# Kernel optimization log

Measured on AMD Instinct MI355X. Metric: run time of the kernel, lower is better.

The kernel has to match this reference:

```python
import math
import jax, jax.numpy as jnp
import numpy as np

B, T, C, H = 2, 2048, 1024, 16

def setup_inputs() -> dict:
    key = jax.random.key(0)
    k1, k2, k3 = jax.random.split(key, 3)
    x = jax.random.normal(k1, (B, T, C), dtype=jnp.float32)
    W_kqv = jax.random.normal(k2, (C, 3 * C), dtype=jnp.float32) * (1.0 / math.sqrt(C))
    W_proj = jax.random.normal(k3, (C, C), dtype=jnp.float32) * (1.0 / math.sqrt(C))
    b_proj = jnp.zeros((C,), dtype=jnp.float32)
    return {"x": x, "W_kqv": W_kqv, "W_proj": W_proj, "b_proj": b_proj}

def reference(x, W_kqv, W_proj, b_proj):
    Bx, Tx, Cx = x.shape
    hs = Cx // H  # head size
    q, k, v = jnp.split(x @ W_kqv, 3, axis=2)  # each (B,T,C)
    # (B,T,C) -> (B,H,T,hs)
    q = q.reshape(Bx, Tx, H, hs).transpose(0, 2, 1, 3)
    k = k.reshape(Bx, Tx, H, hs).transpose(0, 2, 1, 3)
    v = v.reshape(Bx, Tx, H, hs).transpose(0, 2, 1, 3)
    attn = jnp.einsum('bhqd,bhkd->bhqk', q, k) / math.sqrt(hs)  # (B,H,T,T)
    causal = jnp.tril(jnp.ones((Tx, Tx), dtype=bool))
    attn = jnp.where(causal, attn, -jnp.inf)
    attn = jax.nn.softmax(attn, axis=-1)
    y = jnp.einsum('bhqk,bhkd->bhqd', attn, v)  # (B,H,T,hs)
    y = y.transpose(0, 2, 1, 3).reshape(Bx, Tx, Cx)
    return y @ W_proj + b_proj
```

## Files before the change

### kernel.cpp

```cpp
#include <hip/hip_runtime.h>


typedef unsigned short u16;
typedef unsigned int u32;
typedef __bf16 bf16x8 __attribute__((ext_vector_type(8)));
typedef float f32x4 __attribute__((ext_vector_type(4)));
typedef u32 u32x4 __attribute__((ext_vector_type(4)));
typedef u16 u16x4 __attribute__((ext_vector_type(4)));

__constant__ signed char JM[22] = {9,8,7,15,15,14,14,6,13,13,12,12,5,11,11,10,10,4,3,2,1,0};
__constant__ signed char JH[22] = {0,0,0,1, 2, 1, 2, 0,1, 2, 1, 2, 0,1, 2, 1, 2, 0,0,0,0,0};

__device__ __forceinline__ u16 f2bf(float f) {
  u32 u = __float_as_uint(f);
  u32 r = u + 0x7FFFu + ((u >> 16) & 1u);
  return (u16)(r >> 16);
}

__device__ __forceinline__ bf16x8 ld_bf8(const u16* p) {
  union { u32x4 u; bf16x8 b; } x;
  x.u = *(const u32x4*)p;
  return x.b;
}

__device__ __forceinline__ void gld_lds16(const u16* g, u16* l) {
  __builtin_amdgcn_global_load_lds(
      (const __attribute__((address_space(1))) u32*)g,
      (__attribute__((address_space(3))) u32*)l, 16, 0, 0);
}

__global__ __launch_bounds__(256) void conv_x_kernel(const float* __restrict__ src,
                                                     u16* __restrict__ dst) {
  int idx = blockIdx.x * 256 + threadIdx.x;
  const float4* s4 = (const float4*)src;
  float4 a = s4[2 * idx], b = s4[2 * idx + 1];
  union { u16 h[8]; u32x4 v; } pk;
  pk.h[0] = f2bf(a.x); pk.h[1] = f2bf(a.y); pk.h[2] = f2bf(a.z); pk.h[3] = f2bf(a.w);
  pk.h[4] = f2bf(b.x); pk.h[5] = f2bf(b.y); pk.h[6] = f2bf(b.z); pk.h[7] = f2bf(b.w);
  *(u32x4*)&dst[(size_t)idx * 8] = pk.v;
}

__global__ __launch_bounds__(256) void convT_kernel(const float* __restrict__ src,
                                                    u16* __restrict__ dst, int R, int Cc) {
  __shared__ float ls[64][65];
  int r0 = blockIdx.x * 64, c0 = blockIdx.y * 64;
  int t = threadIdx.x;
  for (int u = t; u < 1024; u += 256) {
    int r = u >> 4, cs = (u & 15) << 2;
    float4 v = *(const float4*)&src[(size_t)(r0 + r) * Cc + (c0 + cs)];
    ls[r][cs] = v.x; ls[r][cs + 1] = v.y; ls[r][cs + 2] = v.z; ls[r][cs + 3] = v.w;
  }
  __syncthreads();
  for (int u = t; u < 1024; u += 256) {
    int n = u >> 4, ks = (u & 15) << 2;
    u16x4 o;
    o.x = f2bf(ls[ks][n]); o.y = f2bf(ls[ks + 1][n]);
    o.z = f2bf(ls[ks + 2][n]); o.w = f2bf(ls[ks + 3][n]);
    *(u16x4*)&dst[(size_t)(c0 + n) * R + (r0 + ks)] = o;
  }
}

__global__ __launch_bounds__(256) void qkv_gemm_kernel(
    const u16* __restrict__ A, const u16* __restrict__ Bt,
    u16* __restrict__ Qh, u16* __restrict__ Kh, u16* __restrict__ Vh, float qscale) {
  constexpr int K = 1024;
  __shared__ __align__(16) u16 As[128 * 32];
  __shared__ __align__(16) u16 Bs[128 * 32];
  int t = threadIdx.x;
  int wave = t >> 6, lane = t & 63, quad = lane >> 4, l16 = lane & 15;
  int wm = (wave >> 1) << 6, wn = (wave & 1) << 6;
  int m0 = blockIdx.x * 128, n0 = blockIdx.y * 128;
  f32x4 acc[4][4] = {};
  int u0 = t, u1 = t + 256;
  int ra0 = u0 >> 2, ca0 = ((u0 & 3) ^ ((u0 >> 3) & 3)) << 3;
  int ra1 = u1 >> 2, ca1 = ((u1 & 3) ^ ((u1 >> 3) & 3)) << 3;
  int swq = (quad ^ ((l16 >> 1) & 3)) << 3;
  for (int k0 = 0; k0 < K; k0 += 32) {
    gld_lds16(&A[(size_t)(m0 + ra0) * K + k0 + ca0], &As[u0 * 8]);
    gld_lds16(&A[(size_t)(m0 + ra1) * K + k0 + ca1], &As[u1 * 8]);
    gld_lds16(&Bt[(size_t)(n0 + ra0) * K + k0 + ca0], &Bs[u0 * 8]);
    gld_lds16(&Bt[(size_t)(n0 + ra1) * K + k0 + ca1], &Bs[u1 * 8]);
    __syncthreads();
    bf16x8 af[4], bfr[4];
    for (int r = 0; r < 4; ++r) af[r] = ld_bf8(&As[(wm + r * 16 + l16) * 32 + swq]);
    for (int c = 0; c < 4; ++c) bfr[c] = ld_bf8(&Bs[(wn + c * 16 + l16) * 32 + swq]);
    for (int r = 0; r < 4; ++r)
      for (int c = 0; c < 4; ++c)
        acc[r][c] = __builtin_amdgcn_mfma_f32_16x16x32_bf16(af[r], bfr[c], acc[r][c], 0, 0, 0);
    __syncthreads();
  }
  for (int r = 0; r < 4; ++r) {
    int rowbase = m0 + wm + r * 16 + quad * 4;
    for (int c = 0; c < 4; ++c) {
      int col = n0 + wn + c * 16 + l16;
      int seg = col >> 10;
      int cc = col & 1023;
      int h = cc >> 6, d = cc & 63;
      for (int i = 0; i < 4; ++i) {
        int row = rowbase + i;
        int b = row >> 11, tt = row & 2047;
        size_t off = (((size_t)(b * 16 + h)) * 2048 + tt) * 64 + d;
        float v = acc[r][c][i];
        if (seg == 0)      Qh[off] = f2bf(v * qscale);
        else if (seg == 1) Kh[off] = f2bf(v);
        else               Vh[off] = f2bf(v);
      }
    }
  }
}

__global__ __launch_bounds__(256) void vT_kernel(const u16* __restrict__ Vh,
                                                 u16* __restrict__ Vt) {
  __shared__ __align__(16) u16 ls[64 * 72];
  int t = threadIdx.x;
  int t0 = blockIdx.x * 64, bh = blockIdx.y;
  const u16* in = Vh + ((size_t)bh * 2048 + t0) * 64;
  for (int u = t; u < 512; u += 256) {
    int row = u >> 3, col = (u & 7) << 3;
    *(u32x4*)&ls[row * 72 + col] = *(const u32x4*)&in[(size_t)row * 64 + col];
  }
  __syncthreads();
  for (int u = t; u < 512; u += 256) {
    int d = u >> 3, tc = (u & 7) << 3;
    union { u16 h[8]; u32x4 v; } pk;
    for (int j = 0; j < 8; ++j) pk.h[j] = ls[(tc + j) * 72 + d];
    *(u32x4*)&Vt[((size_t)bh * 64 + d) * 2048 + t0 + tc] = pk.v;
  }
}

__global__ __launch_bounds__(512) void proj_gemm_kernel(
    const u16* __restrict__ A, const u16* __restrict__ Bt,
    float* __restrict__ out, const float* __restrict__ bias) {
  constexpr int K = 1024;
  __shared__ __align__(16) u16 As[128 * 32];
  __shared__ __align__(16) u16 Bs[128 * 32];
  int t = threadIdx.x;
  int wave = t >> 6, lane = t & 63, quad = lane >> 4, l16 = lane & 15;
  int wm = (wave >> 2) << 6, wn = (wave & 3) << 5;
  int m0 = blockIdx.x * 128, n0 = blockIdx.y * 128;
  f32x4 acc[4][2] = {};
  int u0 = t;
  int ra0 = u0 >> 2, ca0 = ((u0 & 3) ^ ((u0 >> 3) & 3)) << 3;
  int swq = (quad ^ ((l16 >> 1) & 3)) << 3;
  for (int k0 = 0; k0 < K; k0 += 32) {
    gld_lds16(&A[(size_t)(m0 + ra0) * K + k0 + ca0], &As[u0 * 8]);
    gld_lds16(&Bt[(size_t)(n0 + ra0) * K + k0 + ca0], &Bs[u0 * 8]);
    __syncthreads();
    bf16x8 af[4], bfr[2];
    for (int r = 0; r < 4; ++r) af[r] = ld_bf8(&As[(wm + r * 16 + l16) * 32 + swq]);
    for (int c = 0; c < 2; ++c) bfr[c] = ld_bf8(&Bs[(wn + c * 16 + l16) * 32 + swq]);
    for (int r = 0; r < 4; ++r)
      for (int c = 0; c < 2; ++c)
        acc[r][c] = __builtin_amdgcn_mfma_f32_16x16x32_bf16(af[r], bfr[c], acc[r][c], 0, 0, 0);
    __syncthreads();
  }
  for (int r = 0; r < 4; ++r) {
    int rowbase = m0 + wm + r * 16 + quad * 4;
    for (int c = 0; c < 2; ++c) {
      int col = n0 + wn + c * 16 + l16;
      float bv = bias[col];
      for (int i = 0; i < 4; ++i)
        out[(size_t)(rowbase + i) * 1024 + col] = acc[r][c][i] + bv;
    }
  }
}

__global__ __launch_bounds__(256) void flash_kernel(
    const u16* __restrict__ Qh, const u16* __restrict__ Kh, const u16* __restrict__ Vt,
    u16* __restrict__ yb, float* __restrict__ Opart) {
  __shared__ __align__(16) u16 Ks[64 * 64];
  __shared__ __align__(16) u16 Vs[64 * 64];
  __shared__ __align__(16) u16 Ps[128 * 64];
  int t = threadIdx.x, wave = t >> 6, lane = t & 63, quad = lane >> 4, l16 = lane & 15;
  int jx = blockIdx.x, bh = blockIdx.y;
  int m = JM[jx], jh = JH[jx];
  int kvs = (jh == 2) ? (m + 1) : 0;
  int kve = (jh == 1) ? (m + 1) : (2 * m + 2);
  bool partial = jh != 0;
  int q0 = m << 7;
  const u16* Qb = Qh + (size_t)bh * 2048 * 64;
  const u16* Kb = Kh + (size_t)bh * 2048 * 64;
  const u16* Vb = Vt + (size_t)bh * 64 * 2048;
  bf16x8 qa[2][2];
  for (int s = 0; s < 2; ++s) {
    int qrow = q0 + wave * 32 + s * 16 + l16;
    qa[s][0] = ld_bf8(&Qb[(size_t)qrow * 64 + quad * 8]);
    qa[s][1] = ld_bf8(&Qb[(size_t)qrow * 64 + 32 + quad * 8]);
  }
  f32x4 oacc[2][4] = {};
  float ls0 = 0.f, ls1 = 0.f;
  int ua = t, ub = t + 256;
  int ra = ua >> 3, cba = ua & 7, rb = ub >> 3, cbb = ub & 7;
  int lka = ra * 64 + ((cba + ra) & 7) * 8;
  int lkb = rb * 64 + ((cbb + rb) & 7) * 8;
  u32x4 kreg0, kreg1, vreg0, vreg1;
  {
    int kv0 = kvs << 6;
    kreg0 = *(const u32x4*)&Kb[(size_t)(kv0 + ra) * 64 + cba * 8];
    kreg1 = *(const u32x4*)&Kb[(size_t)(kv0 + rb) * 64 + cbb * 8];
    vreg0 = *(const u32x4*)&Vb[(size_t)ra * 2048 + kv0 + cba * 8];
    vreg1 = *(const u32x4*)&Vb[(size_t)rb * 2048 + kv0 + cbb * 8];
  }
  for (int j = kvs; j < kve; ++j) {
    int kv0 = j << 6;
    __syncthreads();
    *(u32x4*)&Ks[lka] = kreg0;
    *(u32x4*)&Ks[lkb] = kreg1;
    *(u32x4*)&Vs[lka] = vreg0;
    *(u32x4*)&Vs[lkb] = vreg1;
    __syncthreads();
    if (j + 1 < kve) {
      int kn = (j + 1) << 6;
      kreg0 = *(const u32x4*)&Kb[(size_t)(kn + ra) * 64 + cba * 8];
      kreg1 = *(const u32x4*)&Kb[(size_t)(kn + rb) * 64 + cbb * 8];
      vreg0 = *(const u32x4*)&Vb[(size_t)ra * 2048 + kn + cba * 8];
      vreg1 = *(const u32x4*)&Vb[(size_t)rb * 2048 + kn + cbb * 8];
    }
    bool maskit = (j >= 2 * m);
    for (int c = 0; c < 4; ++c) {
      int krow = c * 16 + l16;
      bf16x8 kb0 = ld_bf8(&Ks[krow * 64 + ((quad + krow) & 7) * 8]);
      bf16x8 kb1 = ld_bf8(&Ks[krow * 64 + ((quad + 4 + krow) & 7) * 8]);
      for (int s = 0; s < 2; ++s) {
        f32x4 z = {0.f, 0.f, 0.f, 0.f};
        z = __builtin_amdgcn_mfma_f32_16x16x32_bf16(kb0, qa[s][0], z, 0, 0, 0);
        z = __builtin_amdgcn_mfma_f32_16x16x32_bf16(kb1, qa[s][1], z, 0, 0, 0);
        int prow = wave * 32 + s * 16 + l16;
        union { u16 hh[4]; u16x4 v; } pk;
        float lsadd = 0.f;
        for (int i = 0; i < 4; ++i) {
          float p = __builtin_amdgcn_exp2f(z[i]);
          if (maskit && (kv0 + c * 16 + quad * 4 + i > q0 + prow)) p = 0.f;
          lsadd += p;
          pk.hh[i] = f2bf(p);
        }
        if (s) ls1 += lsadd; else ls0 += lsadd;
        *(u16x4*)&Ps[prow * 64 + ((2 * c + (quad >> 1) + prow) & 7) * 8 + (quad & 1) * 4] = pk.v;
      }
    }
    bf16x8 pa[2][2];
    for (int s = 0; s < 2; ++s) {
      int prow = wave * 32 + s * 16 + l16;
      pa[s][0] = ld_bf8(&Ps[prow * 64 + ((quad + prow) & 7) * 8]);
      pa[s][1] = ld_bf8(&Ps[prow * 64 + ((quad + 4 + prow) & 7) * 8]);
    }
    for (int dt = 0; dt < 4; ++dt) {
      int vrow = dt * 16 + l16;
      bf16x8 vb0 = ld_bf8(&Vs[vrow * 64 + ((quad + vrow) & 7) * 8]);
      bf16x8 vb1 = ld_bf8(&Vs[vrow * 64 + ((quad + 4 + vrow) & 7) * 8]);
      for (int s = 0; s < 2; ++s) {
        oacc[s][dt] = __builtin_amdgcn_mfma_f32_16x16x32_bf16(pa[s][0], vb0, oacc[s][dt], 0, 0, 0);
        oacc[s][dt] = __builtin_amdgcn_mfma_f32_16x16x32_bf16(pa[s][1], vb1, oacc[s][dt], 0, 0, 0);
      }
    }
  }
  ls0 += __shfl_xor(ls0, 16); ls0 += __shfl_xor(ls0, 32);
  ls1 += __shfl_xor(ls1, 16); ls1 += __shfl_xor(ls1, 32);
  if (partial) {
    float* Op = Opart + ((size_t)(bh * 6 + (m - 10)) * 2 + (jh - 1)) * 8320;
    for (int s = 0; s < 2; ++s)
      for (int dt = 0; dt < 4; ++dt)
        for (int i = 0; i < 4; ++i)
          Op[(wave * 32 + s * 16 + quad * 4 + i) * 64 + dt * 16 + l16] = oacc[s][dt][i];
    if (quad == 0) {
      Op[8192 + wave * 32 + l16] = ls0;
      Op[8192 + wave * 32 + 16 + l16] = ls1;
    }
  } else {
    int b = bh >> 4, hh = bh & 15;
    for (int s = 0; s < 2; ++s) {
      float lss = s ? ls1 : ls0;
      for (int i = 0; i < 4; ++i) {
        float inv = 1.0f / __shfl(lss, quad * 4 + i);
        int qq = q0 + wave * 32 + s * 16 + quad * 4 + i;
        size_t rowoff = ((size_t)(b * 2048 + qq)) * 1024 + hh * 64;
        for (int dt = 0; dt < 4; ++dt)
          yb[rowoff + dt * 16 + l16] = f2bf(oacc[s][dt][i] * inv);
      }
    }
  }
}

__global__ __launch_bounds__(256) void combine_kernel(const float* __restrict__ Opart,
                                                      u16* __restrict__ yb) {
  int sx = blockIdx.x, bh = blockIdx.y, t = threadIdx.x;
  int m = 10 + sx;
  const float* A = Opart + (size_t)(bh * 6 + sx) * 2 * 8320;
  const float* Bp = A + 8320;
  int q = t >> 1, d0 = (t & 1) << 5;
  float inv = 1.0f / (A[8192 + q] + Bp[8192 + q]);
  int b = bh >> 4, h = bh & 15;
  size_t off = ((size_t)(b * 2048 + (m << 7) + q)) * 1024 + h * 64 + d0;
  for (int k0 = 0; k0 < 32; k0 += 8) {
    union { u16 hh[8]; u32x4 v; } pk;
    for (int k = 0; k < 8; ++k)
      pk.hh[k] = f2bf((A[q * 64 + d0 + k0 + k] + Bp[q * 64 + d0 + k0 + k]) * inv);
    *(u32x4*)&yb[off + k0] = pk.v;
  }
}

extern "C" void kernel_launch(void* const* d_in, const int* in_sizes, int n_in,
                              void* d_out, int out_size, void* d_ws, size_t ws_size,
                              hipStream_t stream) {
  const float* x     = (const float*)d_in[0];
  const float* Wkqv  = (const float*)d_in[1];
  const float* Wproj = (const float*)d_in[2];
  const float* bproj = (const float*)d_in[3];
  float* out = (float*)d_out;

  u16* ws     = (u16*)d_ws;
  u16* xb     = ws;
  u16* wkqvT  = xb + (size_t)4096 * 1024;
  u16* wprojT = wkqvT + (size_t)3072 * 1024;
  u16* Qh     = wprojT + (size_t)1024 * 1024;
  u16* Kh     = Qh + (size_t)32 * 2048 * 64;
  u16* Vt     = Kh + (size_t)32 * 2048 * 64;
  u16* yb     = Vt + (size_t)32 * 2048 * 64;
  u16* Vh     = yb;
  float* Opart = (float*)ws;

  const float QSCALE = 0.18033688011112042f;

  conv_x_kernel<<<2048, 256, 0, stream>>>(x, xb);
  convT_kernel<<<dim3(16, 48), 256, 0, stream>>>(Wkqv, wkqvT, 1024, 3072);
  convT_kernel<<<dim3(16, 16), 256, 0, stream>>>(Wproj, wprojT, 1024, 1024);
  qkv_gemm_kernel<<<dim3(32, 24), 256, 0, stream>>>(xb, wkqvT, Qh, Kh, Vh, QSCALE);
  vT_kernel<<<dim3(32, 32), 256, 0, stream>>>(Vh, Vt);
  flash_kernel<<<dim3(22, 32), 256, 0, stream>>>(Qh, Kh, Vt, yb, Opart);
  combine_kernel<<<dim3(6, 32), 256, 0, stream>>>(Opart, yb);
  proj_gemm_kernel<<<dim3(32, 8), 512, 0, stream>>>(yb, wprojT, out, bproj);
}
```

Measured before the change: 198.7 us.

## Split flash attention into single-wave 16-row query blocks with direct global K/V loads

The flash kernel moves from 256-thread blocks over 128 query rows, which staged K/V through shared memory with double-buffered registers, to 64-thread single-wave blocks over 16 query rows. Each wave loads K and V fragments straight from global memory, and the longest 64 row tiles are split in half along the KV axis, with a resized combine kernel merging the halves. The aim is finer load balancing over the causal triangle, no block-level barriers, and more concurrent blocks. In exchange, K/V global traffic rises sharply because each 16-row block re-reads its full K/V prefix without shared-memory reuse, and the global loads are no longer prefetched ahead of use.

```diff
diff --git a/kernel.cpp b/kernel.cpp
--- a/kernel.cpp
+++ b/kernel.cpp
@@ -7,9 +7,6 @@
 typedef float f32x4 __attribute__((ext_vector_type(4)));
 typedef u32 u32x4 __attribute__((ext_vector_type(4)));
 typedef u16 u16x4 __attribute__((ext_vector_type(4)));
-
-__constant__ signed char JM[22] = {9,8,7,15,15,14,14,6,13,13,12,12,5,11,11,10,10,4,3,2,1,0};
-__constant__ signed char JH[22] = {0,0,0,1, 2, 1, 2, 0,1, 2, 1, 2, 0,1, 2, 1, 2, 0,0,0,0,0};
 
 __device__ __forceinline__ u16 f2bf(float f) {
   u32 u = __float_as_uint(f);
@@ -165,138 +162,102 @@
   }
 }
 
-__global__ __launch_bounds__(256) void flash_kernel(
+__global__ __launch_bounds__(64, 4) void flash_kernel(
     const u16* __restrict__ Qh, const u16* __restrict__ Kh, const u16* __restrict__ Vt,
     u16* __restrict__ yb, float* __restrict__ Opart) {
-  __shared__ __align__(16) u16 Ks[64 * 64];
-  __shared__ __align__(16) u16 Vs[64 * 64];
-  __shared__ __align__(16) u16 Ps[128 * 64];
-  int t = threadIdx.x, wave = t >> 6, lane = t & 63, quad = lane >> 4, l16 = lane & 15;
+  __shared__ __align__(16) u16 Ps[16 * 64];
+  int t = threadIdx.x, quad = t >> 4, l16 = t & 15;
   int jx = blockIdx.x, bh = blockIdx.y;
-  int m = JM[jx], jh = JH[jx];
-  int kvs = (jh == 2) ? (m + 1) : 0;
-  int kve = (jh == 1) ? (m + 1) : (2 * m + 2);
-  bool partial = jh != 0;
-  int q0 = m << 7;
+  int s, kvs, kve, half = 0;
+  bool partial = false;
+  if (jx < 32) {
+    s = 95 - jx; kvs = 0; kve = (s >> 2) + 1;
+  } else if (jx < 96) {
+    int idx = jx - 32;
+    s = 96 + (idx >> 1); half = idx & 1;
+    int n = (s >> 2) + 1, mid = n >> 1;
+    kvs = half ? mid : 0; kve = half ? n : mid;
+    partial = true;
+  } else {
+    s = 159 - jx; kvs = 0; kve = (s >> 2) + 1;
+  }
+  int q0 = s << 4, smax = s >> 2;
   const u16* Qb = Qh + (size_t)bh * 2048 * 64;
   const u16* Kb = Kh + (size_t)bh * 2048 * 64;
   const u16* Vb = Vt + (size_t)bh * 64 * 2048;
-  bf16x8 qa[2][2];
-  for (int s = 0; s < 2; ++s) {
-    int qrow = q0 + wave * 32 + s * 16 + l16;
-    qa[s][0] = ld_bf8(&Qb[(size_t)qrow * 64 + quad * 8]);
-    qa[s][1] = ld_bf8(&Qb[(size_t)qrow * 64 + 32 + quad * 8]);
-  }
-  f32x4 oacc[2][4] = {};
-  float ls0 = 0.f, ls1 = 0.f;
-  int ua = t, ub = t + 256;
-  int ra = ua >> 3, cba = ua & 7, rb = ub >> 3, cbb = ub & 7;
-  int lka = ra * 64 + ((cba + ra) & 7) * 8;
-  int lkb = rb * 64 + ((cbb + rb) & 7) * 8;
-  u32x4 kreg0, kreg1, vreg0, vreg1;
-  {
-    int kv0 = kvs << 6;
-    kreg0 = *(const u32x4*)&Kb[(size_t)(kv0 + ra) * 64 + cba * 8];
-    kreg1 = *(const u32x4*)&Kb[(size_t)(kv0 + rb) * 64 + cbb * 8];
-    vreg0 = *(const u32x4*)&Vb[(size_t)ra * 2048 + kv0 + cba * 8];
-    vreg1 = *(const u32x4*)&Vb[(size_t)rb * 2048 + kv0 + cbb * 8];
-  }
+  bf16x8 qa0 = ld_bf8(&Qb[(size_t)(q0 + l16) * 64 + quad * 8]);
+  bf16x8 qa1 = ld_bf8(&Qb[(size_t)(q0 + l16) * 64 + 32 + quad * 8]);
+  f32x4 oacc[4] = {};
+  float lsum = 0.f;
   for (int j = kvs; j < kve; ++j) {
     int kv0 = j << 6;
-    __syncthreads();
-    *(u32x4*)&Ks[lka] = kreg0;
-    *(u32x4*)&Ks[lkb] = kreg1;
-    *(u32x4*)&Vs[lka] = vreg0;
-    *(u32x4*)&Vs[lkb] = vreg1;
-    __syncthreads();
-    if (j + 1 < kve) {
-      int kn = (j + 1) << 6;
-      kreg0 = *(const u32x4*)&Kb[(size_t)(kn + ra) * 64 + cba * 8];
-      kreg1 = *(const u32x4*)&Kb[(size_t)(kn + rb) * 64 + cbb * 8];
-      vreg0 = *(const u32x4*)&Vb[(size_t)ra * 2048 + kn + cba * 8];
-      vreg1 = *(const u32x4*)&Vb[(size_t)rb * 2048 + kn + cbb * 8];
-    }
-    bool maskit = (j >= 2 * m);
+    bf16x8 kb[4][2], vb[4][2];
     for (int c = 0; c < 4; ++c) {
-      int krow = c * 16 + l16;
-      bf16x8 kb0 = ld_bf8(&Ks[krow * 64 + ((quad + krow) & 7) * 8]);
-      bf16x8 kb1 = ld_bf8(&Ks[krow * 64 + ((quad + 4 + krow) & 7) * 8]);
-      for (int s = 0; s < 2; ++s) {
-        f32x4 z = {0.f, 0.f, 0.f, 0.f};
-        z = __builtin_amdgcn_mfma_f32_16x16x32_bf16(kb0, qa[s][0], z, 0, 0, 0);
-        z = __builtin_amdgcn_mfma_f32_16x16x32_bf16(kb1, qa[s][1], z, 0, 0, 0);
-        int prow = wave * 32 + s * 16 + l16;
-        union { u16 hh[4]; u16x4 v; } pk;
-        float lsadd = 0.f;
-        for (int i = 0; i < 4; ++i) {
-          float p = __builtin_amdgcn_exp2f(z[i]);
-          if (maskit && (kv0 + c * 16 + quad * 4 + i > q0 + prow)) p = 0.f;
-          lsadd += p;
-          pk.hh[i] = f2bf(p);
-        }
-        if (s) ls1 += lsadd; else ls0 += lsadd;
-        *(u16x4*)&Ps[prow * 64 + ((2 * c + (quad >> 1) + prow) & 7) * 8 + (quad & 1) * 4] = pk.v;
+      const u16* kp = &Kb[(size_t)(kv0 + c * 16 + l16) * 64 + quad * 8];
+      kb[c][0] = ld_bf8(kp);
+      kb[c][1] = ld_bf8(kp + 32);
+    }
+    for (int dt = 0; dt < 4; ++dt) {
+      const u16* vp = &Vb[(size_t)(dt * 16 + l16) * 2048 + kv0 + quad * 8];
+      vb[dt][0] = ld_bf8(vp);
+      vb[dt][1] = ld_bf8(vp + 32);
+    }
+    bool maskit = (j == smax);
+    for (int c = 0; c < 4; ++c) {
+      f32x4 z = {0.f, 0.f, 0.f, 0.f};
+      z = __builtin_amdgcn_mfma_f32_16x16x32_bf16(kb[c][0], qa0, z, 0, 0, 0);
+      z = __builtin_amdgcn_mfma_f32_16x16x32_bf16(kb[c][1], qa1, z, 0, 0, 0);
+      union { u16 hh[4]; u16x4 v; } pk;
+      for (int i = 0; i < 4; ++i) {
+        float p = __builtin_amdgcn_exp2f(z[i]);
+        if (maskit && (kv0 + c * 16 + quad * 4 + i > q0 + l16)) p = 0.f;
+        lsum += p;
+        pk.hh[i] = f2bf(p);
       }
-    }
-    bf16x8 pa[2][2];
-    for (int s = 0; s < 2; ++s) {
-      int prow = wave * 32 + s * 16 + l16;
-      pa[s][0] = ld_bf8(&Ps[prow * 64 + ((quad + prow) & 7) * 8]);
-      pa[s][1] = ld_bf8(&Ps[prow * 64 + ((quad + 4 + prow) & 7) * 8]);
-    }
+      *(u16x4*)&Ps[l16 * 64 + ((2 * c + (quad >> 1) + l16) & 7) * 8 + (quad & 1) * 4] = pk.v;
+    }
+    bf16x8 pa0 = ld_bf8(&Ps[l16 * 64 + ((quad + l16) & 7) * 8]);
+    bf16x8 pa1 = ld_bf8(&Ps[l16 * 64 + ((quad + 4 + l16) & 7) * 8]);
     for (int dt = 0; dt < 4; ++dt) {
-      int vrow = dt * 16 + l16;
-      bf16x8 vb0 = ld_bf8(&Vs[vrow * 64 + ((quad + vrow) & 7) * 8]);
-      bf16x8 vb1 = ld_bf8(&Vs[vrow * 64 + ((quad + 4 + vrow) & 7) * 8]);
-      for (int s = 0; s < 2; ++s) {
-        oacc[s][dt] = __builtin_amdgcn_mfma_f32_16x16x32_bf16(pa[s][0], vb0, oacc[s][dt], 0, 0, 0);
-        oacc[s][dt] = __builtin_amdgcn_mfma_f32_16x16x32_bf16(pa[s][1], vb1, oacc[s][dt], 0, 0, 0);
-      }
-    }
-  }
-  ls0 += __shfl_xor(ls0, 16); ls0 += __shfl_xor(ls0, 32);
-  ls1 += __shfl_xor(ls1, 16); ls1 += __shfl_xor(ls1, 32);
+      oacc[dt] = __builtin_amdgcn_mfma_f32_16x16x32_bf16(pa0, vb[dt][0], oacc[dt], 0, 0, 0);
+      oacc[dt] = __builtin_amdgcn_mfma_f32_16x16x32_bf16(pa1, vb[dt][1], oacc[dt], 0, 0, 0);
+    }
+  }
+  lsum += __shfl_xor(lsum, 16);
+  lsum += __shfl_xor(lsum, 32);
   if (partial) {
-    float* Op = Opart + ((size_t)(bh * 6 + (m - 10)) * 2 + (jh - 1)) * 8320;
-    for (int s = 0; s < 2; ++s)
+    float* Op = Opart + ((size_t)(bh * 32 + (s - 96)) * 2 + half) * 1040;
+    for (int dt = 0; dt < 4; ++dt)
+      for (int i = 0; i < 4; ++i)
+        Op[(quad * 4 + i) * 64 + dt * 16 + l16] = oacc[dt][i];
+    if (quad == 0) Op[1024 + l16] = lsum;
+  } else {
+    int b = bh >> 4, h = bh & 15;
+    for (int i = 0; i < 4; ++i) {
+      float inv = 1.0f / __shfl(lsum, quad * 4 + i);
+      int qq = q0 + quad * 4 + i;
+      size_t rowoff = ((size_t)(b * 2048 + qq)) * 1024 + h * 64;
       for (int dt = 0; dt < 4; ++dt)
-        for (int i = 0; i < 4; ++i)
-          Op[(wave * 32 + s * 16 + quad * 4 + i) * 64 + dt * 16 + l16] = oacc[s][dt][i];
-    if (quad == 0) {
-      Op[8192 + wave * 32 + l16] = ls0;
-      Op[8192 + wave * 32 + 16 + l16] = ls1;
-    }
-  } else {
-    int b = bh >> 4, hh = bh & 15;
-    for (int s = 0; s < 2; ++s) {
-      float lss = s ? ls1 : ls0;
-      for (int i = 0; i < 4; ++i) {
-        float inv = 1.0f / __shfl(lss, quad * 4 + i);
-        int qq = q0 + wave * 32 + s * 16 + quad * 4 + i;
-        size_t rowoff = ((size_t)(b * 2048 + qq)) * 1024 + hh * 64;
-        for (int dt = 0; dt < 4; ++dt)
-          yb[rowoff + dt * 16 + l16] = f2bf(oacc[s][dt][i] * inv);
-      }
-    }
-  }
-}
-
-__global__ __launch_bounds__(256) void combine_kernel(const float* __restrict__ Opart,
-                                                      u16* __restrict__ yb) {
+        yb[rowoff + dt * 16 + l16] = f2bf(oacc[dt][i] * inv);
+    }
+  }
+}
+
+__global__ __launch_bounds__(64) void combine_kernel(const float* __restrict__ Opart,
+                                                     u16* __restrict__ yb) {
   int sx = blockIdx.x, bh = blockIdx.y, t = threadIdx.x;
-  int m = 10 + sx;
-  const float* A = Opart + (size_t)(bh * 6 + sx) * 2 * 8320;
-  const float* Bp = A + 8320;
-  int q = t >> 1, d0 = (t & 1) << 5;
-  float inv = 1.0f / (A[8192 + q] + Bp[8192 + q]);
+  int s = 96 + sx;
+  const float* A = Opart + (size_t)(bh * 32 + sx) * 2 * 1040;
+  const float* Bp = A + 1040;
+  int r = t >> 2, d0 = (t & 3) << 4;
+  float inv = 1.0f / (A[1024 + r] + Bp[1024 + r]);
   int b = bh >> 4, h = bh & 15;
-  size_t off = ((size_t)(b * 2048 + (m << 7) + q)) * 1024 + h * 64 + d0;
-  for (int k0 = 0; k0 < 32; k0 += 8) {
-    union { u16 hh[8]; u32x4 v; } pk;
-    for (int k = 0; k < 8; ++k)
-      pk.hh[k] = f2bf((A[q * 64 + d0 + k0 + k] + Bp[q * 64 + d0 + k0 + k]) * inv);
-    *(u32x4*)&yb[off + k0] = pk.v;
-  }
+  size_t off = ((size_t)(b * 2048 + (s << 4) + r)) * 1024 + h * 64 + d0;
+  union { u16 hh[16]; u32x4 v[2]; } pk;
+  for (int k = 0; k < 16; ++k)
+    pk.hh[k] = f2bf((A[r * 64 + d0 + k] + Bp[r * 64 + d0 + k]) * inv);
+  *(u32x4*)&yb[off] = pk.v[0];
+  *(u32x4*)&yb[off + 8] = pk.v[1];
 }
 
 extern "C" void kernel_launch(void* const* d_in, const int* in_sizes, int n_in,
@@ -326,7 +287,7 @@
   convT_kernel<<<dim3(16, 16), 256, 0, stream>>>(Wproj, wprojT, 1024, 1024);
   qkv_gemm_kernel<<<dim3(32, 24), 256, 0, stream>>>(xb, wkqvT, Qh, Kh, Vh, QSCALE);
   vT_kernel<<<dim3(32, 32), 256, 0, stream>>>(Vh, Vt);
-  flash_kernel<<<dim3(22, 32), 256, 0, stream>>>(Qh, Kh, Vt, yb, Opart);
-  combine_kernel<<<dim3(6, 32), 256, 0, stream>>>(Opart, yb);
+  flash_kernel<<<dim3(160, 32), 64, 0, stream>>>(Qh, Kh, Vt, yb, Opart);
+  combine_kernel<<<dim3(32, 32), 64, 0, stream>>>(Opart, yb);
   proj_gemm_kernel<<<dim3(32, 8), 512, 0, stream>>>(yb, wprojT, out, bproj);
 }
```

Measured after the change: 288.0 us. +45.0%, slower.
